# Performance work log

Hardware: AMD Instinct MI355X
Metric: run time of the kernel (lower is better)

The kernel has to match this reference:

```python
import jax, jax.numpy as jnp
import numpy as np

L, ND, ED, AD = 2, 128, 64, 64
N, E, A, G = 50000, 300000, 600000, 16
EPS = 1e-5


def _graph_norm(h, batch, num_graphs, w, b):
    # PyG LayerNorm(mode='graph'): scalar mean/var over all nodes*features per graph.
    F = h.shape[-1]
    cnt = jax.ops.segment_sum(jnp.ones(h.shape[0], h.dtype), batch, num_segments=num_graphs)
    norm = jnp.maximum(cnt, 1.0) * F  # [G]
    mean = (jax.ops.segment_sum(h, batch, num_segments=num_graphs).sum(-1) / norm)[batch][:, None]
    hc = h - mean
    var = (jax.ops.segment_sum(hc * hc, batch, num_segments=num_graphs).sum(-1) / norm)
    out = hc * jax.lax.rsqrt(var + EPS)[batch][:, None]
    return out * w + b


def setup_inputs() -> dict:
    key = jax.random.key(0)
    ks = jax.random.split(key, 24)

    def lin(k, fi, fo):
        return jax.random.normal(k, (L, fi, fo), jnp.float32) / jnp.sqrt(float(fi))

    inp = {
        "x": jax.random.normal(ks[0], (N, ND), jnp.float32),
        "edge_attr": jax.random.normal(ks[1], (E, ED), jnp.float32),
        "angle_attr": jax.random.normal(ks[2], (A, AD), jnp.float32),
        # node_edge_mlp: [2*ND+ED -> ED], plain linear (plain_last=True)
        "W_ne": lin(ks[3], 2 * ND + ED, ED), "b_ne": jnp.zeros((L, ED), jnp.float32),
        "g_e": jnp.ones((L, ED), jnp.float32), "be_e": jnp.zeros((L, ED), jnp.float32),
        # edge_angle_mlp: [2*ED+AD -> AD]
        "W_ea": lin(ks[4], 2 * ED + AD, AD), "b_ea": jnp.zeros((L, AD), jnp.float32),
        "g_a": jnp.ones((L, AD), jnp.float32), "be_a": jnp.zeros((L, AD), jnp.float32),
        # edge_graph_mp message net: [2*ED+AD -> ED]
        "W_emp": lin(ks[5], 2 * ED + AD, ED), "b_emp": jnp.zeros((L, ED), jnp.float32),
        "g_emp": jnp.ones((L, ED), jnp.float32), "be_emp": jnp.zeros((L, ED), jnp.float32),
        # node_graph_mp message net: [2*ND+ED -> ND]
        "W_nmp": lin(ks[6], 2 * ND + ED, ND), "b_nmp": jnp.zeros((L, ND), jnp.float32),
        "g_nmp": jnp.ones((L, ND), jnp.float32), "be_nmp": jnp.zeros((L, ND), jnp.float32),
        "node_batch": jnp.sort(jax.random.randint(ks[7], (N,), 0, G)),
        "edge_index": jax.random.randint(ks[8], (2, E), 0, N),
        "edge_batch": jnp.sort(jax.random.randint(ks[9], (E,), 0, G)),
        "threebody_index": jax.random.randint(ks[10], (2, A), 0, E),
        "angle_batch": jnp.sort(jax.random.randint(ks[11], (A,), 0, G)),
        "num_graphs": G,
    }
    return inp


def reference(x, edge_attr, angle_attr,
              W_ne, b_ne, g_e, be_e,
              W_ea, b_ea, g_a, be_a,
              W_emp, b_emp, g_emp, be_emp,
              W_nmp, b_nmp, g_nmp, be_nmp,
              node_batch, edge_index, edge_batch,
              threebody_index, angle_batch, num_graphs):
    src_e, dst_e = edge_index[0], edge_index[1]
    src_t, dst_t = threebody_index[0], threebody_index[1]
    n_nodes, n_edges = x.shape[0], edge_attr.shape[0]
    for i in range(W_ne.shape[0]):
        # node-pair -> edge update + residual + graph norm
        ecat = jnp.concatenate([x[src_e], x[dst_e], edge_attr], axis=-1)
        edge_attr = edge_attr + ecat @ W_ne[i] + b_ne[i]
        edge_attr = _graph_norm(edge_attr, edge_batch, num_graphs, g_e[i], be_e[i])
        # edge-pair -> angle update + residual + graph norm
        acat = jnp.concatenate([edge_attr[src_t], edge_attr[dst_t], angle_attr], axis=-1)
        angle_attr = angle_attr + acat @ W_ea[i] + b_ea[i]
        angle_attr = _graph_norm(angle_attr, angle_batch, num_graphs, g_a[i], be_a[i])
        # edge_graph_mp: angle-mediated message passing over edges
        mcat = jnp.concatenate([edge_attr[src_t], edge_attr[dst_t], angle_attr], axis=-1)
        msg = jax.nn.relu(mcat @ W_emp[i] + b_emp[i])
        agg = jax.ops.segment_sum(msg, dst_t, num_segments=n_edges)
        edge_attr = _graph_norm(edge_attr + agg, edge_batch, num_graphs, g_emp[i], be_emp[i])
        # node_graph_mp: edge-mediated message passing over nodes
        ncat = jnp.concatenate([x[src_e], x[dst_e], edge_attr], axis=-1)
        nmsg = jax.nn.relu(ncat @ W_nmp[i] + b_nmp[i])
        nagg = jax.ops.segment_sum(nmsg, dst_e, num_segments=n_nodes)
        x = _graph_norm(x + nagg, node_batch, num_graphs, g_nmp[i], be_nmp[i])
    return x
```

## Files before the change

kernel.cpp:

```cpp
#include <hip/hip_runtime.h>

typedef __attribute__((ext_vector_type(8))) short bf16x8_t;
typedef __attribute__((ext_vector_type(4))) short bf16x4_t;
typedef __attribute__((ext_vector_type(4))) float f32x4_t;

constexpr int NG = 16;
constexpr float EPS = 1e-5f;

__device__ inline unsigned short f2bf(float f) {
  unsigned u = __builtin_bit_cast(unsigned, f);
  u += 0x7FFFu + ((u >> 16) & 1u);
  return (unsigned short)(u >> 16);
}
__device__ inline float bf2f(unsigned short u) {
  unsigned x = ((unsigned)u) << 16;
  return __builtin_bit_cast(float, x);
}

template<bool F32>
__device__ inline void ldrow8(const void* base, size_t off, float v[8]) {
  if constexpr (F32) {
    const float* p = (const float*)base + off;
    float4 f0 = *(const float4*)p, f1 = *(const float4*)(p + 4);
    v[0]=f0.x; v[1]=f0.y; v[2]=f0.z; v[3]=f0.w;
    v[4]=f1.x; v[5]=f1.y; v[6]=f1.z; v[7]=f1.w;
  } else {
    bf16x8_t t = *(const bf16x8_t*)((const unsigned short*)base + off);
#pragma unroll
    for (int k = 0; k < 8; ++k) v[k] = bf2f((unsigned short)t[k]);
  }
}
template<bool F32>
__device__ inline float ldel(const void* base, size_t off) {
  if constexpr (F32) return ((const float*)base)[off];
  return bf2f(((const unsigned short*)base)[off]);
}

__global__ __launch_bounds__(256) void k_dense_x(
    const float* __restrict__ x,
    const unsigned short* __restrict__ WtNE,
    const unsigned short* __restrict__ WtNM,
    unsigned short* __restrict__ P, int nN)
{
  int gw = (int)((blockIdx.x * 256u + threadIdx.x) >> 6);
  int ntile = nN >> 4;
  if (gw >= ntile) return;
  int lane = threadIdx.x & 63;
  int colb = lane & 15;
  int ko = (lane >> 4) << 3;
  int rowb = (lane >> 4) << 2;
  int row = (gw << 4) + colb;
  const float* xr = x + (size_t)row * 128;
  f32x4_t a1[4] = {}, a2[4] = {}, a3[8] = {}, a4[8] = {};
#pragma unroll
  for (int c = 0; c < 4; ++c) {
    float4 f0 = *(const float4*)(xr + c * 32 + ko);
    float4 f1 = *(const float4*)(xr + c * 32 + ko + 4);
    float vv[8] = {f0.x,f0.y,f0.z,f0.w,f1.x,f1.y,f1.z,f1.w};
    bf16x8_t a;
#pragma unroll
    for (int k = 0; k < 8; ++k) a[k] = (short)f2bf(vv[k]);
#pragma unroll
    for (int nb = 0; nb < 4; ++nb) {
      bf16x8_t b1 = *(const bf16x8_t*)(WtNE + (size_t)(nb * 16 + colb) * 320 + c * 32 + ko);
      a1[nb] = __builtin_amdgcn_mfma_f32_16x16x32_bf16(a, b1, a1[nb], 0, 0, 0);
      bf16x8_t b2 = *(const bf16x8_t*)(WtNE + (size_t)(nb * 16 + colb) * 320 + (c + 4) * 32 + ko);
      a2[nb] = __builtin_amdgcn_mfma_f32_16x16x32_bf16(a, b2, a2[nb], 0, 0, 0);
    }
#pragma unroll
    for (int nb = 0; nb < 8; ++nb) {
      bf16x8_t b3 = *(const bf16x8_t*)(WtNM + (size_t)(nb * 16 + colb) * 320 + c * 32 + ko);
      a3[nb] = __builtin_amdgcn_mfma_f32_16x16x32_bf16(a, b3, a3[nb], 0, 0, 0);
      bf16x8_t b4 = *(const bf16x8_t*)(WtNM + (size_t)(nb * 16 + colb) * 320 + (c + 4) * 32 + ko);
      a4[nb] = __builtin_amdgcn_mfma_f32_16x16x32_bf16(a, b4, a4[nb], 0, 0, 0);
    }
  }
#pragma unroll
  for (int r = 0; r < 4; ++r) {
    size_t ro = (size_t)((gw << 4) + rowb + r) * 384;
    bf16x4_t t1, t2;
#pragma unroll
    for (int nb = 0; nb < 4; ++nb) { t1[nb] = (short)f2bf(a1[nb][r]); t2[nb] = (short)f2bf(a2[nb][r]); }
    *(bf16x4_t*)(P + ro + colb * 4) = t1;
    *(bf16x4_t*)(P + ro + 64 + colb * 4) = t2;
    bf16x8_t t3, t4;
#pragma unroll
    for (int nb = 0; nb < 8; ++nb) { t3[nb] = (short)f2bf(a3[nb][r]); t4[nb] = (short)f2bf(a4[nb][r]); }
    *(bf16x8_t*)(P + ro + 128 + colb * 8) = t3;
    *(bf16x8_t*)(P + ro + 256 + colb * 8) = t4;
  }
}

__global__ __launch_bounds__(256) void k_prep_e(
    const unsigned short* __restrict__ eA, const int* __restrict__ ebatch,
    const float* __restrict__ afA, const float* __restrict__ afB,
    const unsigned short* __restrict__ WtP,
    unsigned short* __restrict__ eB1, unsigned short* __restrict__ PE, int nE)
{
  __shared__ float lA[1024], lB[1024];
  for (int i = threadIdx.x; i < 1024; i += 256) { lA[i] = afA[i]; lB[i] = afB[i]; }
  __syncthreads();
  int gw = (int)((blockIdx.x * 256u + threadIdx.x) >> 6);
  int ntile = nE >> 4;
  if (gw >= ntile) return;
  int lane = threadIdx.x & 63;
  int colb = lane & 15;
  int ko = (lane >> 4) << 3;
  int rowb = (lane >> 4) << 2;
  int row = (gw << 4) + colb;
  int ge = ebatch[row];
  f32x4_t a3[4] = {}, a4[4] = {};
#pragma unroll
  for (int c2 = 0; c2 < 2; ++c2) {
    int fb = c2 * 32 + ko;
    bf16x8_t t = *(const bf16x8_t*)(eA + (size_t)row * 64 + fb);
    bf16x8_t an;
#pragma unroll
    for (int k = 0; k < 8; ++k)
      an[k] = (short)f2bf(bf2f((unsigned short)t[k]) * lA[ge*64 + fb + k] + lB[ge*64 + fb + k]);
    *(bf16x8_t*)(eB1 + (size_t)row * 64 + fb) = an;
#pragma unroll
    for (int nb = 0; nb < 4; ++nb) {
      bf16x8_t b3 = *(const bf16x8_t*)(WtP + (size_t)(nb * 16 + colb) * 192 + c2 * 32 + ko);
      a3[nb] = __builtin_amdgcn_mfma_f32_16x16x32_bf16(an, b3, a3[nb], 0, 0, 0);
      bf16x8_t b4 = *(const bf16x8_t*)(WtP + (size_t)(nb * 16 + colb) * 192 + 64 + c2 * 32 + ko);
      a4[nb] = __builtin_amdgcn_mfma_f32_16x16x32_bf16(an, b4, a4[nb], 0, 0, 0);
    }
  }
#pragma unroll
  for (int r = 0; r < 4; ++r) {
    size_t ro = (size_t)((gw << 4) + rowb + r) * 128;
    bf16x4_t t3, t4;
#pragma unroll
    for (int nb = 0; nb < 4; ++nb) { t3[nb] = (short)f2bf(a3[nb][r]); t4[nb] = (short)f2bf(a4[nb][r]); }
    *(bf16x4_t*)(PE + ro + colb * 4) = t3;
    *(bf16x4_t*)(PE + ro + 64 + colb * 4) = t4;
  }
}

template<bool EF32>
__global__ __launch_bounds__(256) void k_edge(
    const unsigned short* __restrict__ P, const void* e_in, unsigned short* e_out,
    const int* __restrict__ ei, const int* __restrict__ ebatch,
    const unsigned short* __restrict__ Wt,
    const float* __restrict__ bias,
    const float* __restrict__ afA, const float* __restrict__ afB,
    float* __restrict__ gs1, float* __restrict__ gs2,
    unsigned short* __restrict__ pn, int nE)
{
  __shared__ float lA[1024], lB[1024];
  __shared__ float ls1[NG], ls2[NG];
  for (int i = threadIdx.x; i < 1024; i += 256) { lA[i] = afA[i]; lB[i] = afB[i]; }
  if (threadIdx.x < NG) { ls1[threadIdx.x] = 0.f; ls2[threadIdx.x] = 0.f; }
  __syncthreads();
  int gw = (int)((blockIdx.x * 256u + threadIdx.x) >> 6);
  int ntile = nE >> 4;
  bool act = gw < ntile;
  int lane = threadIdx.x & 63;
  int colb = lane & 15;
  int ko = (lane >> 4) << 3;
  int rowb = (lane >> 4) << 2;
  float sr[4] = {0.f,0.f,0.f,0.f}, ssr[4] = {0.f,0.f,0.f,0.f};
  if (act) {
    int sI[4], dI[4];
#pragma unroll
    for (int r = 0; r < 4; ++r) {
      int e_r = (gw << 4) + rowb + r;
      sI[r] = ei[e_r]; dI[r] = ei[nE + e_r];
    }
    bf16x4_t g1[4], g2[4]; bf16x8_t g3[4], g4[4];
#pragma unroll
    for (int r = 0; r < 4; ++r) {
      g1[r] = *(const bf16x4_t*)(P + (size_t)sI[r] * 384 + colb * 4);
      g2[r] = *(const bf16x4_t*)(P + (size_t)dI[r] * 384 + 64 + colb * 4);
      g3[r] = *(const bf16x8_t*)(P + (size_t)sI[r] * 384 + 128 + colb * 8);
      g4[r] = *(const bf16x8_t*)(P + (size_t)dI[r] * 384 + 256 + colb * 8);
    }
    int row = (gw << 4) + colb;
    int ge = ebatch[row];
    f32x4_t acc[4] = {};
#pragma unroll
    for (int c2 = 0; c2 < 2; ++c2) {
      int fb = c2 * 32 + ko;
      float vv[8];
      ldrow8<EF32>(e_in, (size_t)row * 64 + fb, vv);
      bf16x8_t a;
#pragma unroll
      for (int k = 0; k < 8; ++k) a[k] = (short)f2bf(vv[k] * lA[ge*64 + fb + k] + lB[ge*64 + fb + k]);
#pragma unroll
      for (int nb = 0; nb < 4; ++nb) {
        bf16x8_t b = *(const bf16x8_t*)(Wt + (size_t)(nb * 16 + colb) * 320 + (8 + c2) * 32 + ko);
        acc[nb] = __builtin_amdgcn_mfma_f32_16x16x32_bf16(a, b, acc[nb], 0, 0, 0);
      }
    }
#pragma unroll
    for (int r = 0; r < 4; ++r) {
      int e_ = (gw << 4) + rowb + r;
      int gr = ebatch[e_];
#pragma unroll
      for (int nb = 0; nb < 4; ++nb) {
        int col = nb * 16 + colb;
        size_t off = (size_t)e_ * 64 + col;
        float ev = ldel<EF32>(e_in, off);
        float vv = ev * lA[gr*64 + col] + lB[gr*64 + col] + bias[col]
                 + acc[nb][r] + bf2f((unsigned short)g1[r][nb]) + bf2f((unsigned short)g2[r][nb]);
        e_out[off] = f2bf(vv);
        sr[r] += vv; ssr[r] += vv * vv;
      }
      bf16x8_t pv;
#pragma unroll
      for (int k = 0; k < 8; ++k)
        pv[k] = (short)f2bf(bf2f((unsigned short)g3[r][k]) + bf2f((unsigned short)g4[r][k]));
      *(bf16x8_t*)(pn + (size_t)e_ * 128 + colb * 8) = pv;
    }
  }
#pragma unroll
  for (int m = 1; m <= 8; m <<= 1)
#pragma unroll
    for (int r = 0; r < 4; ++r) { sr[r] += __shfl_xor(sr[r], m); ssr[r] += __shfl_xor(ssr[r], m); }
  if (act && colb == 0) {
#pragma unroll
    for (int r = 0; r < 4; ++r) {
      int g = ebatch[(gw << 4) + rowb + r];
      atomicAdd(&ls1[g], sr[r]); atomicAdd(&ls2[g], ssr[r]);
    }
  }
  __syncthreads();
  if (threadIdx.x < NG) {
    atomicAdd(&gs1[threadIdx.x], ls1[threadIdx.x]);
    atomicAdd(&gs2[threadIdx.x], ls2[threadIdx.x]);
  }
}

template<bool AF32>
__global__ __launch_bounds__(256) void k_angle(
    const unsigned short* __restrict__ eB1, const unsigned short* __restrict__ PE,
    const void* a_in, unsigned short* a_out,
    const int* __restrict__ ti, const int* __restrict__ abatch,
    const unsigned short* __restrict__ Wt, const float* __restrict__ bias,
    const float* __restrict__ afAA, const float* __restrict__ afAB,
    float* __restrict__ gs1, float* __restrict__ gs2,
    unsigned short* __restrict__ pe, int nA)
{
  __shared__ float lAA[1024], lAB[1024];
  __shared__ float ls1[NG], ls2[NG];
  for (int i = threadIdx.x; i < 1024; i += 256) { lAA[i] = afAA[i]; lAB[i] = afAB[i]; }
  if (threadIdx.x < NG) { ls1[threadIdx.x] = 0.f; ls2[threadIdx.x] = 0.f; }
  __syncthreads();
  int gw = (int)((blockIdx.x * 256u + threadIdx.x) >> 6);
  int ntile = nA >> 4;
  bool act = gw < ntile;
  int lane = threadIdx.x & 63;
  int colb = lane & 15;
  int ko = (lane >> 4) << 3;
  int rowb = (lane >> 4) << 2;
  float sr[4] = {0.f,0.f,0.f,0.f}, ssr[4] = {0.f,0.f,0.f,0.f};
  if (act) {
    int sI[4], dI[4];
#pragma unroll
    for (int r = 0; r < 4; ++r) {
      int a_r = (gw << 4) + rowb + r;
      sI[r] = ti[a_r]; dI[r] = ti[nA + a_r];
    }
    bf16x4_t g3[4], g4[4];
#pragma unroll
    for (int r = 0; r < 4; ++r) {
      g3[r] = *(const bf16x4_t*)(PE + (size_t)sI[r] * 128 + colb * 4);
      g4[r] = *(const bf16x4_t*)(PE + (size_t)dI[r] * 128 + 64 + colb * 4);
    }
    int row = (gw << 4) + colb;
    int s = ti[row], d = ti[nA + row];
    int ga = abatch[row];
    const unsigned short* es = eB1 + (size_t)s * 64;
    const unsigned short* ed = eB1 + (size_t)d * 64;
    f32x4_t acc[4] = {};
#pragma unroll
    for (int c = 0; c < 6; ++c) {
      bf16x8_t a;
      if (c < 4) {
        const unsigned short* bp = (c < 2) ? es + c * 32 : ed + (c - 2) * 32;
        a = *(const bf16x8_t*)(bp + ko);
      } else {
        int fb = (c - 4) * 32 + ko;
        float vv[8];
        ldrow8<AF32>(a_in, (size_t)row * 64 + fb, vv);
#pragma unroll
        for (int k = 0; k < 8; ++k) a[k] = (short)f2bf(vv[k] * lAA[ga*64 + fb + k] + lAB[ga*64 + fb + k]);
      }
#pragma unroll
      for (int nb = 0; nb < 4; ++nb) {
        bf16x8_t b = *(const bf16x8_t*)(Wt + (size_t)(nb * 16 + colb) * 192 + c * 32 + ko);
        acc[nb] = __builtin_amdgcn_mfma_f32_16x16x32_bf16(a, b, acc[nb], 0, 0, 0);
      }
    }
#pragma unroll
    for (int r = 0; r < 4; ++r) {
      int a_ = (gw << 4) + rowb + r;
      int gr = abatch[a_];
#pragma unroll
      for (int nb = 0; nb < 4; ++nb) {
        int col = nb * 16 + colb;
        size_t off = (size_t)a_ * 64 + col;
        float av = ldel<AF32>(a_in, off);
        float vv = av * lAA[gr*64 + col] + lAB[gr*64 + col] + bias[col] + acc[nb][r];
        a_out[off] = f2bf(vv);
        sr[r] += vv; ssr[r] += vv * vv;
      }
      bf16x4_t pv;
#pragma unroll
      for (int nb = 0; nb < 4; ++nb)
        pv[nb] = (short)f2bf(bf2f((unsigned short)g3[r][nb]) + bf2f((unsigned short)g4[r][nb]));
      *(bf16x4_t*)(pe + (size_t)a_ * 64 + colb * 4) = pv;
    }
  }
#pragma unroll
  for (int m = 1; m <= 8; m <<= 1)
#pragma unroll
    for (int r = 0; r < 4; ++r) { sr[r] += __shfl_xor(sr[r], m); ssr[r] += __shfl_xor(ssr[r], m); }
  if (act && colb == 0) {
#pragma unroll
    for (int r = 0; r < 4; ++r) {
      int g = abatch[(gw << 4) + rowb + r];
      atomicAdd(&ls1[g], sr[r]); atomicAdd(&ls2[g], ssr[r]);
    }
  }
  __syncthreads();
  if (threadIdx.x < NG) {
    atomicAdd(&gs1[threadIdx.x], ls1[threadIdx.x]);
    atomicAdd(&gs2[threadIdx.x], ls2[threadIdx.x]);
  }
}

__global__ __launch_bounds__(256) void k_fin_emp(
    const unsigned short* __restrict__ a_, const int* __restrict__ abatch,
    const unsigned short* __restrict__ Wt,
    const float* __restrict__ bias,
    const float* __restrict__ afAA, const float* __restrict__ afAB,
    unsigned short* __restrict__ msg, int nA)
{
  __shared__ float lAA[1024], lAB[1024];
  for (int i = threadIdx.x; i < 1024; i += 256) { lAA[i] = afAA[i]; lAB[i] = afAB[i]; }
  __syncthreads();
  int gw = (int)((blockIdx.x * 256u + threadIdx.x) >> 6);
  int ntile = nA >> 4;
  if (gw >= ntile) return;
  int lane = threadIdx.x & 63;
  int colb = lane & 15;
  int ko = (lane >> 4) << 3;
  int rowb = (lane >> 4) << 2;
  int row = (gw << 4) + colb;
  int ga = abatch[row];
  f32x4_t acc[4] = {};
#pragma unroll
  for (int c2 = 0; c2 < 2; ++c2) {
    int fb = c2 * 32 + ko;
    bf16x8_t t = *(const bf16x8_t*)(a_ + (size_t)row * 64 + fb);
    bf16x8_t a;
#pragma unroll
    for (int k = 0; k < 8; ++k)
      a[k] = (short)f2bf(bf2f((unsigned short)t[k]) * lAA[ga*64 + fb + k] + lAB[ga*64 + fb + k]);
#pragma unroll
    for (int nb = 0; nb < 4; ++nb) {
      bf16x8_t b = *(const bf16x8_t*)(Wt + (size_t)(nb * 16 + colb) * 192 + 128 + c2 * 32 + ko);
      acc[nb] = __builtin_amdgcn_mfma_f32_16x16x32_bf16(a, b, acc[nb], 0, 0, 0);
    }
  }
  bf16x4_t p4[4];
#pragma unroll
  for (int r = 0; r < 4; ++r)
    p4[r] = *(const bf16x4_t*)(msg + (size_t)((gw << 4) + rowb + r) * 64 + colb * 4);
#pragma unroll
  for (int r = 0; r < 4; ++r) {
    int a_idx = (gw << 4) + rowb + r;
#pragma unroll
    for (int nb = 0; nb < 4; ++nb) {
      int col = nb * 16 + colb;
      float v = fmaxf(acc[nb][r] + bf2f((unsigned short)p4[r][nb]) + bias[col], 0.f);
      msg[(size_t)a_idx * 64 + col] = f2bf(v);
    }
  }
}

__global__ __launch_bounds__(256) void k_fin_nmp(
    const unsigned short* __restrict__ e, const int* __restrict__ ebatch,
    const unsigned short* __restrict__ Wt,
    const float* __restrict__ bias,
    const float* __restrict__ afEA, const float* __restrict__ afEB,
    const unsigned short* __restrict__ pn,
    unsigned short* __restrict__ msg, int nE)
{
  __shared__ float lEA[1024], lEB[1024];
  for (int i = threadIdx.x; i < 1024; i += 256) { lEA[i] = afEA[i]; lEB[i] = afEB[i]; }
  __syncthreads();
  int gw = (int)((blockIdx.x * 256u + threadIdx.x) >> 6);
  int ntile = nE >> 4;
  if (gw >= ntile) return;
  int lane = threadIdx.x & 63;
  int colb = lane & 15;
  int ko = (lane >> 4) << 3;
  int rowb = (lane >> 4) << 2;
  int row = (gw << 4) + colb;
  int ge = ebatch[row];
  f32x4_t acc[8] = {};
#pragma unroll
  for (int c2 = 0; c2 < 2; ++c2) {
    int fb = c2 * 32 + ko;
    bf16x8_t t = *(const bf16x8_t*)(e + (size_t)row * 64 + fb);
    bf16x8_t a;
#pragma unroll
    for (int k = 0; k < 8; ++k)
      a[k] = (short)f2bf(bf2f((unsigned short)t[k]) * lEA[ge*64 + fb + k] + lEB[ge*64 + fb + k]);
#pragma unroll
    for (int nb = 0; nb < 8; ++nb) {
      bf16x8_t b = *(const bf16x8_t*)(Wt + (size_t)(nb * 16 + colb) * 320 + (8 + c2) * 32 + ko);
      acc[nb] = __builtin_amdgcn_mfma_f32_16x16x32_bf16(a, b, acc[nb], 0, 0, 0);
    }
  }
#pragma unroll
  for (int r = 0; r < 4; ++r) {
    int e_ = (gw << 4) + rowb + r;
    bf16x8_t p8 = *(const bf16x8_t*)(pn + (size_t)e_ * 128 + colb * 8);
#pragma unroll
    for (int nb = 0; nb < 8; ++nb) {
      int col = nb * 16 + colb;
      float v = fmaxf(acc[nb][r] + bf2f((unsigned short)p8[nb]) + bias[col], 0.f);
      msg[(size_t)e_ * 128 + col] = f2bf(v);
    }
  }
}

__global__ __launch_bounds__(256) void k_red_e(
    const unsigned short* __restrict__ msg, const unsigned short* e_in, unsigned short* e_out,
    const int* __restrict__ ptr, const int* __restrict__ perm,
    const int* __restrict__ ebatch,
    const float* __restrict__ afA, const float* __restrict__ afB,
    float* __restrict__ gs1, float* __restrict__ gs2, int nE)
{
  __shared__ float lA[1024], lB[1024], ls1[NG], ls2[NG];
  for (int i = threadIdx.x; i < 1024; i += 256) { lA[i] = afA[i]; lB[i] = afB[i]; }
  if (threadIdx.x < NG) { ls1[threadIdx.x] = 0.f; ls2[threadIdx.x] = 0.f; }
  __syncthreads();
  int lane = threadIdx.x & 63;
  int wv = (int)((blockIdx.x * 256u + threadIdx.x) >> 6);
  int nw = (int)((gridDim.x * 256u) >> 6);
  for (int eidx = wv; eidx < nE; eidx += nw) {
    int p0 = ptr[eidx], p1 = ptr[eidx + 1];
    float sum = 0.f;
    for (int j = p0; j < p1; ++j) {
      int aidx = perm[j];
      sum += bf2f(msg[(size_t)aidx * 64 + lane]);
    }
    int g = ebatch[eidx];
    size_t off = (size_t)eidx * 64 + lane;
    float v = bf2f(e_in[off]) * lA[g*64 + lane] + lB[g*64 + lane] + sum;
    e_out[off] = f2bf(v);
    float s = v, ss = v * v;
#pragma unroll
    for (int m = 1; m < 64; m <<= 1) { s += __shfl_xor(s, m); ss += __shfl_xor(ss, m); }
    if (lane == 0) { atomicAdd(&ls1[g], s); atomicAdd(&ls2[g], ss); }
  }
  __syncthreads();
  if (threadIdx.x < NG) {
    atomicAdd(&gs1[threadIdx.x], ls1[threadIdx.x]);
    atomicAdd(&gs2[threadIdx.x], ls2[threadIdx.x]);
  }
}

__global__ __launch_bounds__(256) void k_red_n(
    const unsigned short* __restrict__ msg, const float* x_in, float* out,
    const int* __restrict__ ptr, const int* __restrict__ perm,
    const int* __restrict__ nbatch,
    float* __restrict__ gs1, float* __restrict__ gs2, int nN)
{
  __shared__ float ls1[NG], ls2[NG];
  if (threadIdx.x < NG) { ls1[threadIdx.x] = 0.f; ls2[threadIdx.x] = 0.f; }
  __syncthreads();
  int lane = threadIdx.x & 63;
  int wv = (int)((blockIdx.x * 256u + threadIdx.x) >> 6);
  int nw = (int)((gridDim.x * 256u) >> 6);
  for (int n = wv; n < nN; n += nw) {
    int p0 = ptr[n], p1 = ptr[n + 1];
    float s0 = 0.f, s1v = 0.f;
    for (int j = p0; j < p1; ++j) {
      int e = perm[j];
      unsigned u = *(const unsigned*)(msg + (size_t)e * 128 + lane * 2);
      s0 += bf2f((unsigned short)(u & 0xffffu));
      s1v += bf2f((unsigned short)(u >> 16));
    }
    size_t off = (size_t)n * 128 + lane * 2;
    float h0 = x_in[off] + s0, h1 = x_in[off + 1] + s1v;
    out[off] = h0; out[off + 1] = h1;
    float s = h0 + h1, ss = h0 * h0 + h1 * h1;
#pragma unroll
    for (int m = 1; m < 64; m <<= 1) { s += __shfl_xor(s, m); ss += __shfl_xor(ss, m); }
    if (lane == 0) { int g = nbatch[n]; atomicAdd(&ls1[g], s); atomicAdd(&ls2[g], ss); }
  }
  __syncthreads();
  if (threadIdx.x < NG) {
    atomicAdd(&gs1[threadIdx.x], ls1[threadIdx.x]);
    atomicAdd(&gs2[threadIdx.x], ls2[threadIdx.x]);
  }
}

__global__ __launch_bounds__(256) void k_mkaff(
    const float* __restrict__ s1, const float* __restrict__ s2,
    const float* __restrict__ cnt, int F,
    const float* __restrict__ w, const float* __restrict__ b,
    float* __restrict__ A, float* __restrict__ B)
{
  int idx = blockIdx.x * 256 + threadIdx.x;
  if (idx >= NG * F) return;
  int g = idx / F, f = idx - g * F;
  float norm = fmaxf(cnt[g], 1.f) * (float)F;
  float m = s1[g] / norm;
  float var = s2[g] / norm - m * m;
  float inv = rsqrtf(var + EPS);
  float a = inv * w[f];
  A[idx] = a;
  B[idx] = b[f] - m * a;
}

__global__ __launch_bounds__(256) void k_idaff(float* __restrict__ A, float* __restrict__ B, int n)
{
  int idx = blockIdx.x * 256 + threadIdx.x;
  if (idx < n) { A[idx] = 1.f; B[idx] = 0.f; }
}

__global__ __launch_bounds__(256) void k_apply(
    float* h, const int* __restrict__ batch,
    const float* __restrict__ A, const float* __restrict__ B, int nN)
{
  int total = nN * 16;
  int stride = gridDim.x * 256;
  for (int idx = blockIdx.x * 256 + threadIdx.x; idx < total; idx += stride) {
    int row = idx >> 4, q = (idx & 15) * 8;
    int g = batch[row];
    float* hp = h + (size_t)row * 128 + q;
    float4 f0 = *(const float4*)hp;
    float4 f1 = *(const float4*)(hp + 4);
    float vv[8] = {f0.x,f0.y,f0.z,f0.w,f1.x,f1.y,f1.z,f1.w};
#pragma unroll
    for (int k = 0; k < 8; ++k) vv[k] = vv[k] * A[(g << 7) + q + k] + B[(g << 7) + q + k];
    float4 g0 = {vv[0],vv[1],vv[2],vv[3]}, g1 = {vv[4],vv[5],vv[6],vv[7]};
    *(float4*)hp = g0;
    *(float4*)(hp + 4) = g1;
  }
}

__global__ __launch_bounds__(256) void k_count(
    const int* __restrict__ batch, int n, float* __restrict__ cnt)
{
  __shared__ float lc[NG];
  if (threadIdx.x < NG) lc[threadIdx.x] = 0.f;
  __syncthreads();
  for (int i = blockIdx.x * 256 + threadIdx.x; i < n; i += gridDim.x * 256)
    atomicAdd(&lc[batch[i]], 1.f);
  __syncthreads();
  if (threadIdx.x < NG) atomicAdd(&cnt[threadIdx.x], lc[threadIdx.x]);
}

__global__ __launch_bounds__(256) void k_hist(
    const int* __restrict__ dst, int n, int* __restrict__ cnt)
{
  for (int i = blockIdx.x * 256 + threadIdx.x; i < n; i += gridDim.x * 256)
    atomicAdd(&cnt[dst[i]], 1);
}

__global__ __launch_bounds__(256) void k_scan1(
    const int* __restrict__ in, int* __restrict__ out, int* __restrict__ bsum, int n)
{
  __shared__ int wtot[4];
  int tid = threadIdx.x, lane = tid & 63, wid = tid >> 6;
  int base = blockIdx.x * 1024 + tid * 4;
  int v[4];
#pragma unroll
  for (int k = 0; k < 4; ++k) v[k] = (base + k < n) ? in[base + k] : 0;
  int tsum = v[0] + v[1] + v[2] + v[3];
  int incl = tsum;
#pragma unroll
  for (int off = 1; off < 64; off <<= 1) {
    int up = __shfl_up(incl, off);
    if (lane >= off) incl += up;
  }
  if (lane == 63) wtot[wid] = incl;
  __syncthreads();
  if (tid == 0) {
    int r = 0;
#pragma unroll
    for (int w2 = 0; w2 < 4; ++w2) { int t = wtot[w2]; wtot[w2] = r; r += t; }
    bsum[blockIdx.x] = r;
  }
  __syncthreads();
  int excl = wtot[wid] + incl - tsum;
#pragma unroll
  for (int k = 0; k < 4; ++k) {
    if (base + k < n) out[base + k] = excl;
    excl += v[k];
  }
}

__global__ __launch_bounds__(256) void k_scan2(int* __restrict__ bsum, int nb, int* __restrict__ total_out)
{
  __shared__ int wtot[4];
  int tid = threadIdx.x, lane = tid & 63, wid = tid >> 6;
  int base = tid * 4;
  int v[4];
#pragma unroll
  for (int k = 0; k < 4; ++k) v[k] = (base + k < nb) ? bsum[base + k] : 0;
  int tsum = v[0] + v[1] + v[2] + v[3];
  int incl = tsum;
#pragma unroll
  for (int off = 1; off < 64; off <<= 1) {
    int up = __shfl_up(incl, off);
    if (lane >= off) incl += up;
  }
  if (lane == 63) wtot[wid] = incl;
  __syncthreads();
  if (tid == 0) {
    int r = 0;
#pragma unroll
    for (int w2 = 0; w2 < 4; ++w2) { int t = wtot[w2]; wtot[w2] = r; r += t; }
    *total_out = r;
  }
  __syncthreads();
  int excl = wtot[wid] + incl - tsum;
#pragma unroll
  for (int k = 0; k < 4; ++k) {
    if (base + k < nb) bsum[base + k] = excl;
    excl += v[k];
  }
}

__global__ __launch_bounds__(256) void k_scan3(
    int* __restrict__ ptr, int* __restrict__ cur, const int* __restrict__ bsum, int n)
{
  for (int i = blockIdx.x * 256 + threadIdx.x; i < n; i += gridDim.x * 256) {
    int v = ptr[i] + bsum[i >> 10];
    ptr[i] = v; cur[i] = v;
  }
}

__global__ __launch_bounds__(256) void k_scatter(
    const int* __restrict__ dst, int* __restrict__ cur, int* __restrict__ perm, int n)
{
  for (int i = blockIdx.x * 256 + threadIdx.x; i < n; i += gridDim.x * 256) {
    int d = dst[i];
    int p = atomicAdd(&cur[d], 1);
    perm[p] = i;
  }
}

__global__ __launch_bounds__(256) void k_wt(
    const float* __restrict__ W, unsigned short* __restrict__ Wt, int K, int NO)
{
  int idx = blockIdx.x * 256 + threadIdx.x;
  if (idx >= K * NO) return;
  int k = idx / NO, j = idx - k * NO;
  Wt[(size_t)j * K + k] = f2bf(W[idx]);
}

extern "C" void kernel_launch(void* const* d_in, const int* in_sizes, int n_in,
                              void* d_out, int out_size, void* d_ws, size_t ws_size,
                              hipStream_t stream)
{
  const float* x0    = (const float*)d_in[0];
  const float* e0    = (const float*)d_in[1];
  const float* a0    = (const float*)d_in[2];
  const float* W_ne  = (const float*)d_in[3];
  const float* b_ne  = (const float*)d_in[4];
  const float* g_e   = (const float*)d_in[5];
  const float* be_e  = (const float*)d_in[6];
  const float* W_ea  = (const float*)d_in[7];
  const float* b_ea  = (const float*)d_in[8];
  const float* g_a   = (const float*)d_in[9];
  const float* be_a  = (const float*)d_in[10];
  const float* W_emp = (const float*)d_in[11];
  const float* b_emp = (const float*)d_in[12];
  const float* g_emp = (const float*)d_in[13];
  const float* be_emp= (const float*)d_in[14];
  const float* W_nmp = (const float*)d_in[15];
  const float* b_nmp = (const float*)d_in[16];
  const float* g_nmp = (const float*)d_in[17];
  const float* be_nmp= (const float*)d_in[18];
  const int* node_batch  = (const int*)d_in[19];
  const int* edge_index  = (const int*)d_in[20];
  const int* edge_batch  = (const int*)d_in[21];
  const int* tb_index    = (const int*)d_in[22];
  const int* angle_batch = (const int*)d_in[23];

  const int N = in_sizes[0] / 128;
  const int E = in_sizes[1] / 64;
  const int A = in_sizes[2] / 64;

  char* wsp = (char*)d_ws;
  auto alloc = [&](size_t bytes) { char* p = wsp; wsp += (bytes + 255) & ~(size_t)255; return p; };
  unsigned short* eAB  = (unsigned short*)alloc((size_t)E * 64 * 2);
  unsigned short* aAB  = (unsigned short*)alloc((size_t)A * 64 * 2);
  unsigned short* msg  = (unsigned short*)alloc((size_t)A * 64 * 2);
  unsigned short* pn   = (unsigned short*)alloc((size_t)E * 128 * 2);
  unsigned short* eB1  = (unsigned short*)alloc((size_t)E * 64 * 2);
  unsigned short* PE   = (unsigned short*)alloc((size_t)E * 128 * 2);
  int* ptr_n  = (int*)alloc((size_t)(N + 1) * 4);
  int* cur_n  = (int*)alloc((size_t)N * 4);
  int* perm_n = (int*)alloc((size_t)E * 4);
  int* ptr_e  = (int*)alloc((size_t)(E + 1) * 4);
  int* cur_e  = (int*)alloc((size_t)E * 4);
  int* perm_e = (int*)alloc((size_t)A * 4);
  int* bsum   = (int*)alloc(4096 * 4);
  float* stats = (float*)alloc(5 * NG * 4);
  float* s1    = stats;
  float* s2    = stats + NG;
  float* cnt_n = stats + 2 * NG;
  float* cnt_e = stats + 3 * NG;
  float* cnt_a = stats + 4 * NG;
  float* afE_idA = (float*)alloc(1024 * 4); float* afE_idB = (float*)alloc(1024 * 4);
  float* afA_idA = (float*)alloc(1024 * 4); float* afA_idB = (float*)alloc(1024 * 4);
  float* afE1A   = (float*)alloc(1024 * 4); float* afE1B   = (float*)alloc(1024 * 4);
  float* afE2A   = (float*)alloc(1024 * 4); float* afE2B   = (float*)alloc(1024 * 4);
  float* afA1A   = (float*)alloc(1024 * 4); float* afA1B   = (float*)alloc(1024 * 4);
  float* afXA    = (float*)alloc(2048 * 4); float* afXB    = (float*)alloc(2048 * 4);
  unsigned short* wt_ne  = (unsigned short*)alloc((size_t)2 * 320 * 64 * 2);
  unsigned short* wt_ea  = (unsigned short*)alloc((size_t)2 * 192 * 64 * 2);
  unsigned short* wt_emp = (unsigned short*)alloc((size_t)2 * 192 * 64 * 2);
  unsigned short* wt_nmp = (unsigned short*)alloc((size_t)2 * 320 * 128 * 2);

  unsigned short* P = msg;
  float* x_out = (float*)d_out;

  for (int i = 0; i < 2; ++i) {
    k_wt<<<(320*64 + 255)/256, 256, 0, stream>>>(W_ne  + (size_t)i*320*64,  wt_ne  + (size_t)i*320*64,  320, 64);
    k_wt<<<(192*64 + 255)/256, 256, 0, stream>>>(W_ea  + (size_t)i*192*64,  wt_ea  + (size_t)i*192*64,  192, 64);
    k_wt<<<(192*64 + 255)/256, 256, 0, stream>>>(W_emp + (size_t)i*192*64,  wt_emp + (size_t)i*192*64,  192, 64);
    k_wt<<<(320*128 + 255)/256, 256, 0, stream>>>(W_nmp + (size_t)i*320*128, wt_nmp + (size_t)i*320*128, 320, 128);
  }
  hipMemsetAsync(stats, 0, 5 * NG * 4, stream);
  k_count<<<512, 256, 0, stream>>>(node_batch, N, cnt_n);
  k_count<<<512, 256, 0, stream>>>(edge_batch, E, cnt_e);
  k_count<<<512, 256, 0, stream>>>(angle_batch, A, cnt_a);
  k_idaff<<<4, 256, 0, stream>>>(afE_idA, afE_idB, 1024);
  k_idaff<<<4, 256, 0, stream>>>(afA_idA, afA_idB, 1024);

  hipMemsetAsync(cur_n, 0, (size_t)N * 4, stream);
  hipMemsetAsync(cur_e, 0, (size_t)E * 4, stream);
  k_hist<<<1024, 256, 0, stream>>>(edge_index + E, E, cur_n);
  k_hist<<<1024, 256, 0, stream>>>(tb_index + A, A, cur_e);
  int nbN = (N + 1023) / 1024, nbE = (E + 1023) / 1024;
  k_scan1<<<nbN, 256, 0, stream>>>(cur_n, ptr_n, bsum, N);
  k_scan2<<<1, 256, 0, stream>>>(bsum, nbN, ptr_n + N);
  k_scan3<<<1024, 256, 0, stream>>>(ptr_n, cur_n, bsum, N);
  k_scatter<<<1024, 256, 0, stream>>>(edge_index + E, cur_n, perm_n, E);
  k_scan1<<<nbE, 256, 0, stream>>>(cur_e, ptr_e, bsum, E);
  k_scan2<<<1, 256, 0, stream>>>(bsum, nbE, ptr_e + E);
  k_scan3<<<1024, 256, 0, stream>>>(ptr_e, cur_e, bsum, E);
  k_scatter<<<1024, 256, 0, stream>>>(tb_index + A, cur_e, perm_e, A);

  const float* x_cur = x0;
  int blkE = (E / 16 + 3) / 4;
  int blkA = (A / 16 + 3) / 4;
  int blkN = (N / 16 + 3) / 4;

  for (int i = 0; i < 2; ++i) {
    const float* fEinA = (i == 0) ? afE_idA : afE2A;
    const float* fEinB = (i == 0) ? afE_idB : afE2B;
    const float* fAinA = (i == 0) ? afA_idA : afA1A;
    const float* fAinB = (i == 0) ? afA_idB : afA1B;

    k_dense_x<<<blkN, 256, 0, stream>>>(x_cur, wt_ne + (size_t)i*320*64,
                                        wt_nmp + (size_t)i*320*128, P, N);

    hipMemsetAsync(s1, 0, 2 * NG * 4, stream);
    if (i == 0)
      k_edge<true><<<blkE, 256, 0, stream>>>(P, (const void*)e0, eAB, edge_index, edge_batch,
                                             wt_ne + (size_t)i*320*64, b_ne + i*64,
                                             fEinA, fEinB, s1, s2, pn, E);
    else
      k_edge<false><<<blkE, 256, 0, stream>>>(P, (const void*)eAB, eAB, edge_index, edge_batch,
                                              wt_ne + (size_t)i*320*64, b_ne + i*64,
                                              fEinA, fEinB, s1, s2, pn, E);
    k_mkaff<<<4, 256, 0, stream>>>(s1, s2, cnt_e, 64, g_e + i*64, be_e + i*64, afE1A, afE1B);

    k_prep_e<<<blkE, 256, 0, stream>>>(eAB, edge_batch, afE1A, afE1B,
                                       wt_emp + (size_t)i*192*64, eB1, PE, E);

    hipMemsetAsync(s1, 0, 2 * NG * 4, stream);
    if (i == 0)
      k_angle<true><<<blkA, 256, 0, stream>>>(eB1, PE, (const void*)a0, aAB, tb_index, angle_batch,
                                              wt_ea + (size_t)i*192*64, b_ea + i*64,
                                              fAinA, fAinB, s1, s2, msg, A);
    else
      k_angle<false><<<blkA, 256, 0, stream>>>(eB1, PE, (const void*)aAB, aAB, tb_index, angle_batch,
                                               wt_ea + (size_t)i*192*64, b_ea + i*64,
                                               fAinA, fAinB, s1, s2, msg, A);
    k_mkaff<<<4, 256, 0, stream>>>(s1, s2, cnt_a, 64, g_a + i*64, be_a + i*64, afA1A, afA1B);

    k_fin_emp<<<blkA, 256, 0, stream>>>(aAB, angle_batch, wt_emp + (size_t)i*192*64,
                                        b_emp + i*64, afA1A, afA1B, msg, A);
    hipMemsetAsync(s1, 0, 2 * NG * 4, stream);
    k_red_e<<<2048, 256, 0, stream>>>(msg, eAB, eAB, ptr_e, perm_e, edge_batch,
                                      afE1A, afE1B, s1, s2, E);
    k_mkaff<<<4, 256, 0, stream>>>(s1, s2, cnt_e, 64, g_emp + i*64, be_emp + i*64, afE2A, afE2B);

    k_fin_nmp<<<blkE, 256, 0, stream>>>(eAB, edge_batch, wt_nmp + (size_t)i*320*128,
                                        b_nmp + i*128, afE2A, afE2B, pn, msg, E);
    hipMemsetAsync(s1, 0, 2 * NG * 4, stream);
    k_red_n<<<2048, 256, 0, stream>>>(msg, x_cur, x_out, ptr_n, perm_n, node_batch,
                                      s1, s2, N);
    k_mkaff<<<8, 256, 0, stream>>>(s1, s2, cnt_n, 128, g_nmp + i*128, be_nmp + i*128, afXA, afXB);
    k_apply<<<2048, 256, 0, stream>>>(x_out, node_batch, afXA, afXB, N);

    x_cur = x_out;
  }
}
```

Baseline: 1.712 ms.

## Precompute edge-side angle projections per edge instead of per angle

```diff
diff --git a/kernel.cpp b/kernel.cpp
--- a/kernel.cpp
+++ b/kernel.cpp
@@ -94,8 +94,9 @@
 __global__ __launch_bounds__(256) void k_prep_e(
     const unsigned short* __restrict__ eA, const int* __restrict__ ebatch,
     const float* __restrict__ afA, const float* __restrict__ afB,
+    const unsigned short* __restrict__ WtA,
     const unsigned short* __restrict__ WtP,
-    unsigned short* __restrict__ eB1, unsigned short* __restrict__ PE, int nE)
+    unsigned short* __restrict__ PAE, int nE)
 {
   __shared__ float lA[1024], lB[1024];
   for (int i = threadIdx.x; i < 1024; i += 256) { lA[i] = afA[i]; lB[i] = afB[i]; }
@@ -109,7 +110,7 @@
   int rowb = (lane >> 4) << 2;
   int row = (gw << 4) + colb;
   int ge = ebatch[row];
-  f32x4_t a3[4] = {}, a4[4] = {};
+  f32x4_t pa1[4] = {}, pa2[4] = {}, pe3[4] = {}, pe4[4] = {};
 #pragma unroll
   for (int c2 = 0; c2 < 2; ++c2) {
     int fb = c2 * 32 + ko;
@@ -118,23 +119,31 @@
 #pragma unroll
     for (int k = 0; k < 8; ++k)
       an[k] = (short)f2bf(bf2f((unsigned short)t[k]) * lA[ge*64 + fb + k] + lB[ge*64 + fb + k]);
-    *(bf16x8_t*)(eB1 + (size_t)row * 64 + fb) = an;
 #pragma unroll
     for (int nb = 0; nb < 4; ++nb) {
-      bf16x8_t b3 = *(const bf16x8_t*)(WtP + (size_t)(nb * 16 + colb) * 192 + c2 * 32 + ko);
-      a3[nb] = __builtin_amdgcn_mfma_f32_16x16x32_bf16(an, b3, a3[nb], 0, 0, 0);
-      bf16x8_t b4 = *(const bf16x8_t*)(WtP + (size_t)(nb * 16 + colb) * 192 + 64 + c2 * 32 + ko);
-      a4[nb] = __builtin_amdgcn_mfma_f32_16x16x32_bf16(an, b4, a4[nb], 0, 0, 0);
+      size_t wb = (size_t)(nb * 16 + colb) * 192;
+      bf16x8_t b;
+      b = *(const bf16x8_t*)(WtA + wb + c2 * 32 + ko);
+      pa1[nb] = __builtin_amdgcn_mfma_f32_16x16x32_bf16(an, b, pa1[nb], 0, 0, 0);
+      b = *(const bf16x8_t*)(WtA + wb + 64 + c2 * 32 + ko);
+      pa2[nb] = __builtin_amdgcn_mfma_f32_16x16x32_bf16(an, b, pa2[nb], 0, 0, 0);
+      b = *(const bf16x8_t*)(WtP + wb + c2 * 32 + ko);
+      pe3[nb] = __builtin_amdgcn_mfma_f32_16x16x32_bf16(an, b, pe3[nb], 0, 0, 0);
+      b = *(const bf16x8_t*)(WtP + wb + 64 + c2 * 32 + ko);
+      pe4[nb] = __builtin_amdgcn_mfma_f32_16x16x32_bf16(an, b, pe4[nb], 0, 0, 0);
     }
   }
 #pragma unroll
   for (int r = 0; r < 4; ++r) {
-    size_t ro = (size_t)((gw << 4) + rowb + r) * 128;
-    bf16x4_t t3, t4;
-#pragma unroll
-    for (int nb = 0; nb < 4; ++nb) { t3[nb] = (short)f2bf(a3[nb][r]); t4[nb] = (short)f2bf(a4[nb][r]); }
-    *(bf16x4_t*)(PE + ro + colb * 4) = t3;
-    *(bf16x4_t*)(PE + ro + 64 + colb * 4) = t4;
+    size_t ro = (size_t)((gw << 4) + rowb + r) * 256;
+    bf16x8_t sH, dH;
+#pragma unroll
+    for (int nb = 0; nb < 4; ++nb) {
+      sH[nb] = (short)f2bf(pa1[nb][r]); sH[4 + nb] = (short)f2bf(pe3[nb][r]);
+      dH[nb] = (short)f2bf(pa2[nb][r]); dH[4 + nb] = (short)f2bf(pe4[nb][r]);
+    }
+    *(bf16x8_t*)(PAE + ro + colb * 8) = sH;
+    *(bf16x8_t*)(PAE + ro + 128 + colb * 8) = dH;
   }
 }
 
@@ -234,10 +243,11 @@
 
 template<bool AF32>
 __global__ __launch_bounds__(256) void k_angle(
-    const unsigned short* __restrict__ eB1, const unsigned short* __restrict__ PE,
+    const unsigned short* __restrict__ PAE,
     const void* a_in, unsigned short* a_out,
     const int* __restrict__ ti, const int* __restrict__ abatch,
-    const unsigned short* __restrict__ Wt, const float* __restrict__ bias,
+    const unsigned short* __restrict__ Wt,
+    const float* __restrict__ bias,
     const float* __restrict__ afAA, const float* __restrict__ afAB,
     float* __restrict__ gs1, float* __restrict__ gs2,
     unsigned short* __restrict__ pe, int nA)
@@ -262,34 +272,26 @@
       int a_r = (gw << 4) + rowb + r;
       sI[r] = ti[a_r]; dI[r] = ti[nA + a_r];
     }
-    bf16x4_t g3[4], g4[4];
+    bf16x8_t gS[4], gD[4];
 #pragma unroll
     for (int r = 0; r < 4; ++r) {
-      g3[r] = *(const bf16x4_t*)(PE + (size_t)sI[r] * 128 + colb * 4);
-      g4[r] = *(const bf16x4_t*)(PE + (size_t)dI[r] * 128 + 64 + colb * 4);
+      gS[r] = *(const bf16x8_t*)(PAE + (size_t)sI[r] * 256 + colb * 8);
+      gD[r] = *(const bf16x8_t*)(PAE + (size_t)dI[r] * 256 + 128 + colb * 8);
     }
     int row = (gw << 4) + colb;
-    int s = ti[row], d = ti[nA + row];
     int ga = abatch[row];
-    const unsigned short* es = eB1 + (size_t)s * 64;
-    const unsigned short* ed = eB1 + (size_t)d * 64;
     f32x4_t acc[4] = {};
 #pragma unroll
-    for (int c = 0; c < 6; ++c) {
+    for (int c2 = 0; c2 < 2; ++c2) {
+      int fb = c2 * 32 + ko;
+      float vv[8];
+      ldrow8<AF32>(a_in, (size_t)row * 64 + fb, vv);
       bf16x8_t a;
-      if (c < 4) {
-        const unsigned short* bp = (c < 2) ? es + c * 32 : ed + (c - 2) * 32;
-        a = *(const bf16x8_t*)(bp + ko);
-      } else {
-        int fb = (c - 4) * 32 + ko;
-        float vv[8];
-        ldrow8<AF32>(a_in, (size_t)row * 64 + fb, vv);
-#pragma unroll
-        for (int k = 0; k < 8; ++k) a[k] = (short)f2bf(vv[k] * lAA[ga*64 + fb + k] + lAB[ga*64 + fb + k]);
-      }
+#pragma unroll
+      for (int k = 0; k < 8; ++k) a[k] = (short)f2bf(vv[k] * lAA[ga*64 + fb + k] + lAB[ga*64 + fb + k]);
 #pragma unroll
       for (int nb = 0; nb < 4; ++nb) {
-        bf16x8_t b = *(const bf16x8_t*)(Wt + (size_t)(nb * 16 + colb) * 192 + c * 32 + ko);
+        bf16x8_t b = *(const bf16x8_t*)(Wt + (size_t)(nb * 16 + colb) * 192 + 128 + c2 * 32 + ko);
         acc[nb] = __builtin_amdgcn_mfma_f32_16x16x32_bf16(a, b, acc[nb], 0, 0, 0);
       }
     }
@@ -302,14 +304,15 @@
         int col = nb * 16 + colb;
         size_t off = (size_t)a_ * 64 + col;
         float av = ldel<AF32>(a_in, off);
-        float vv = av * lAA[gr*64 + col] + lAB[gr*64 + col] + bias[col] + acc[nb][r];
+        float vv = av * lAA[gr*64 + col] + lAB[gr*64 + col] + bias[col] + acc[nb][r]
+                 + bf2f((unsigned short)gS[r][nb]) + bf2f((unsigned short)gD[r][nb]);
         a_out[off] = f2bf(vv);
         sr[r] += vv; ssr[r] += vv * vv;
       }
       bf16x4_t pv;
 #pragma unroll
       for (int nb = 0; nb < 4; ++nb)
-        pv[nb] = (short)f2bf(bf2f((unsigned short)g3[r][nb]) + bf2f((unsigned short)g4[r][nb]));
+        pv[nb] = (short)f2bf(bf2f((unsigned short)gS[r][4 + nb]) + bf2f((unsigned short)gD[r][4 + nb]));
       *(bf16x4_t*)(pe + (size_t)a_ * 64 + colb * 4) = pv;
     }
   }
@@ -698,8 +701,7 @@
   unsigned short* aAB  = (unsigned short*)alloc((size_t)A * 64 * 2);
   unsigned short* msg  = (unsigned short*)alloc((size_t)A * 64 * 2);
   unsigned short* pn   = (unsigned short*)alloc((size_t)E * 128 * 2);
-  unsigned short* eB1  = (unsigned short*)alloc((size_t)E * 64 * 2);
-  unsigned short* PE   = (unsigned short*)alloc((size_t)E * 128 * 2);
+  unsigned short* PAE  = (unsigned short*)alloc((size_t)E * 256 * 2);
   int* ptr_n  = (int*)alloc((size_t)(N + 1) * 4);
   int* cur_n  = (int*)alloc((size_t)N * 4);
   int* perm_n = (int*)alloc((size_t)E * 4);
@@ -780,15 +782,16 @@
     k_mkaff<<<4, 256, 0, stream>>>(s1, s2, cnt_e, 64, g_e + i*64, be_e + i*64, afE1A, afE1B);
 
     k_prep_e<<<blkE, 256, 0, stream>>>(eAB, edge_batch, afE1A, afE1B,
-                                       wt_emp + (size_t)i*192*64, eB1, PE, E);
+                                       wt_ea + (size_t)i*192*64, wt_emp + (size_t)i*192*64,
+                                       PAE, E);
 
     hipMemsetAsync(s1, 0, 2 * NG * 4, stream);
     if (i == 0)
-      k_angle<true><<<blkA, 256, 0, stream>>>(eB1, PE, (const void*)a0, aAB, tb_index, angle_batch,
+      k_angle<true><<<blkA, 256, 0, stream>>>(PAE, (const void*)a0, aAB, tb_index, angle_batch,
                                               wt_ea + (size_t)i*192*64, b_ea + i*64,
                                               fAinA, fAinB, s1, s2, msg, A);
     else
-      k_angle<false><<<blkA, 256, 0, stream>>>(eB1, PE, (const void*)aAB, aAB, tb_index, angle_batch,
+      k_angle<false><<<blkA, 256, 0, stream>>>(PAE, (const void*)aAB, aAB, tb_index, angle_batch,
                                                wt_ea + (size_t)i*192*64, b_ea + i*64,
                                                fAinA, fAinB, s1, s2, msg, A);
     k_mkaff<<<4, 256, 0, stream>>>(s1, s2, cnt_a, 64, g_a + i*64, be_a + i*64, afA1A, afA1B);
```

Measured after the change: 1.681 ms. About the same (-1.8%).
